# Performance work log

Hardware: AMD Instinct MI355X
Metric: run time of the kernel (lower is better)

Reference implementation:

```python
import math
import jax, jax.numpy as jnp
import numpy as np

B, P, L = 32, 128, 64
DIN, TE, H, NH, NL = 16, 64, 512, 8, 2
DH = H // NH
DP = DIN + TE
TAU = 300.0
DELTA = 300.0

_PARAM_SPEC = [
    ("te_scale_w", (1, 1)), ("te_scale_b", (1,)),
    ("te_per_w", (TE - 1, 1)), ("te_per_b", (TE - 1,)),
    ("inp_w", (H, DP)), ("inp_b", (H,)),
    ("wq", (H, H)), ("bq", (H,)), ("wk", (H, H)), ("bk", (H,)),
    ("wv", (H, H)), ("bv", (H,)), ("wo", (H, H)), ("bo", (H,)),
    ("ffn_w1", (H, H)), ("ffn_b1", (H,)), ("ffn_w2", (H, H)), ("ffn_b2", (H,)),
    ("ln1_g", (H,)), ("ln1_b", (H,)), ("ln2_g", (H,)), ("ln2_b", (H,)),
    ("exists_bias", (1, 1, H)),
    ("gwq", (NL, H, H)), ("gbq", (NL, H)), ("gwk", (NL, H, H)), ("gbk", (NL, H)),
    ("gwv", (NL, H, H)), ("gbv", (NL, H)), ("gwo", (NL, H, H)), ("gbo", (NL, H)),
]


def setup_inputs() -> dict:
    key = jax.random.key(0)
    ks = jax.random.split(key, 3 + len(_PARAM_SPEC))
    inp = {
        "x": jax.random.normal(ks[0], (B, P, L, DIN), jnp.float32),
        "tt": jax.random.uniform(ks[1], (B, P, L, 1), jnp.float32),
        "mask": jax.random.randint(ks[2], (B, P, L, 1), 0, 2).astype(jnp.int32),
    }
    for i, (name, shp) in enumerate(_PARAM_SPEC):
        inp[name] = 0.02 * jax.random.normal(ks[3 + i], shp, jnp.float32)
    # LayerNorm affine params: gamma=1, beta=0
    inp["ln1_g"] = jnp.ones((H,), jnp.float32)
    inp["ln1_b"] = jnp.zeros((H,), jnp.float32)
    inp["ln2_g"] = jnp.ones((H,), jnp.float32)
    inp["ln2_b"] = jnp.zeros((H,), jnp.float32)
    return inp


def _layernorm(x, g, b, eps=1e-5):
    m = x.mean(-1, keepdims=True)
    v = ((x - m) ** 2).mean(-1, keepdims=True)
    return (x - m) / jnp.sqrt(v + eps) * g + b


def _time_bias(m):
    idx = jnp.arange(m)
    dist = jnp.abs(idx[:, None] - idx[None, :]).astype(jnp.float32) * DELTA
    return jnp.log(jnp.exp(-dist / TAU) + 1e-12)  # [P, P]


def _pos_encoding(p, d):
    pos = jnp.arange(p, dtype=jnp.float32)[:, None]
    div = jnp.exp(jnp.arange(0, d, 2, dtype=jnp.float32) * (-math.log(10000.0) / d))
    pe = jnp.zeros((p, d), jnp.float32)
    pe = pe.at[:, 0::2].set(jnp.sin(pos * div))
    pe = pe.at[:, 1::2].set(jnp.cos(pos * div))
    return pe


def reference(x, tt, mask,
              te_scale_w, te_scale_b, te_per_w, te_per_b,
              inp_w, inp_b, wq, bq, wk, bk, wv, bv, wo, bo,
              ffn_w1, ffn_b1, ffn_w2, ffn_b2, ln1_g, ln1_b, ln2_g, ln2_b,
              exists_bias, gwq, gbq, gwk, gbk, gwv, gbv, gwo, gbo):
    b, p, l, _ = x.shape
    # --- Learnable time embedding: scale linear + sin(periodic linear), concat ---
    te1 = tt @ te_scale_w.T + te_scale_b                      # [B,P,L,1]
    te2 = jnp.sin(tt @ te_per_w.T + te_per_b)                 # [B,P,L,TE-1]
    pts = jnp.concatenate([x, te1, te2], axis=-1)             # [B,P,L,DP]

    valid = (mask[..., 0] > 0).reshape(b * p, l)              # [N,L] bool
    h = (pts.reshape(b * p, l, DP) @ inp_w.T) + inp_b         # [N,L,H]

    has_any = jnp.any(valid, axis=1)                          # [N]
    key_pad = ~valid
    # Empty patches: unmask position 0 and zero its features
    key_pad = key_pad.at[:, 0].set(key_pad[:, 0] & has_any)
    pos0 = (jnp.arange(l) == 0)[None, :, None]
    h = jnp.where((~has_any)[:, None, None] & pos0, 0.0, h)

    # --- Intra-patch MHA (GAT) ---
    def heads(t, w, bias):
        return ((t @ w.T) + bias).reshape(b * p, l, NH, DH)
    q, k, v = heads(h, wq, bq), heads(h, wk, bk), heads(h, wv, bv)
    sc = jnp.einsum("nqhd,nkhd->nhqk", q, k) / math.sqrt(DH)
    sc = jnp.where(key_pad[:, None, None, :], -1e9, sc)
    z = jnp.einsum("nhqk,nkhd->nqhd", jax.nn.softmax(sc, axis=-1), v)
    z = z.reshape(b * p, l, H) @ wo.T + bo
    h = _layernorm(h + z, ln1_g, ln1_b)
    ffn = jax.nn.relu(h @ ffn_w1.T + ffn_b1) @ ffn_w2.T + ffn_b2
    h = _layernorm(h + ffn, ln2_g, ln2_b)

    # Masked mean pooling -> patch tokens
    w = valid.astype(jnp.float32)[..., None]                  # [N,L,1]
    denom = jnp.clip(w.sum(axis=1), 1.0)
    h = ((h * w).sum(axis=1) / denom).reshape(b, p, H)        # [B,P,H]

    # Exists bias for missing patches + positional encoding
    pexists = has_any.reshape(b, p).astype(jnp.float32)       # [B,P]
    h = h + exists_bias * (1.0 - pexists)[..., None]
    h = h + _pos_encoding(p, H)[None]

    # --- Patch-level time-biased graph attention stack (residual) ---
    tb = _time_bias(p)[None, None]                            # [1,1,P,P]
    kp = (pexists <= 0.0)[:, None, None, :]                   # [B,1,1,P]
    for li in range(NL):
        def gh(t, w, bias):
            return ((t @ w.T) + bias).reshape(b, p, NH, DH)
        q = gh(h, gwq[li], gbq[li])
        k = gh(h, gwk[li], gbk[li])
        v = gh(h, gwv[li], gbv[li])
        att = jnp.einsum("bqhd,bkhd->bhqk", q, k) / math.sqrt(DH) + tb
        att = jnp.where(kp, -1e9, att)
        out = jnp.einsum("bhqk,bkhd->bqhd", jax.nn.softmax(att, axis=-1), v)
        out = out.reshape(b, p, H) @ gwo[li].T + gbo[li]
        out = out * pexists[..., None]
        h = h + out
    return h
```

## Files before the change

### kernel.cpp

```cpp
#include <hip/hip_runtime.h>

#define NTOK 4096
#define CH   512
#define NCHUNK 8

typedef _Float16 f16;
typedef __attribute__((ext_vector_type(8))) _Float16 half8;
typedef __attribute__((ext_vector_type(4))) _Float16 half4;
typedef __attribute__((ext_vector_type(4))) float f32x4;

#define OFF_INPW 0
#define OFF_WQKV (512*128)
#define OFF_WO   (OFF_WQKV + 3*512*512)
#define OFF_W1   (OFF_WO + 512*512)
#define OFF_W2   (OFF_W1 + 512*512)
#define OFF_GW   (OFF_W2 + 512*512)
#define WBF_TOT  (OFF_GW + 8*512*512)

static __device__ __forceinline__ f32x4 mfma16(half8 a, half8 b, f32x4 c){
  return __builtin_amdgcn_mfma_f32_16x16x32_f16(a, b, c, 0, 0, 0);
}

static __device__ __forceinline__ void gld_lds16(const f16* g, f16* l){
  __builtin_amdgcn_global_load_lds(
      (const __attribute__((address_space(1))) void*)g,
      (__attribute__((address_space(3))) void*)l, 16, 0, 0);
}

#define FULL_BARRIER() do { \
    asm volatile("" ::: "memory"); \
    __builtin_amdgcn_s_barrier(); \
    __builtin_amdgcn_sched_barrier(0); \
  } while(0)

__global__ __launch_bounds__(256) void conv_weights(
    const float* __restrict__ inpw, const float* __restrict__ wq, const float* __restrict__ wk,
    const float* __restrict__ wv, const float* __restrict__ wo, const float* __restrict__ w1,
    const float* __restrict__ w2, const float* __restrict__ gwq, const float* __restrict__ gwk,
    const float* __restrict__ gwv, const float* __restrict__ gwo, f16* __restrict__ wbf,
    const float* __restrict__ bq, const float* __restrict__ bk, const float* __restrict__ bv,
    const float* __restrict__ gbq, const float* __restrict__ gbk, const float* __restrict__ gbv,
    float* __restrict__ biasb)
{
  int e = blockIdx.x*256 + threadIdx.x;
  int y = blockIdx.y;
  if (y == 0){
    if (e < 512*128){
      int row = e>>7, col = e&127;
      float v = (col < 80) ? inpw[row*80 + col] : 0.f;
      wbf[OFF_INPW + e] = (f16)v;
    }
    return;
  }
  if (y == 15){
    if (e < 1536){
      biasb[e] = (e < 512) ? bq[e] : (e < 1024 ? bk[e-512] : bv[e-1024]);
    } else if (e < 3*1536){
      int idx = e - 1536, li = idx/1536, c = idx - li*1536;
      float v = (c < 512) ? gbq[li*512 + c] : (c < 1024 ? gbk[li*512 + c-512] : gbv[li*512 + c-1024]);
      biasb[e] = v;
    }
    return;
  }
  if (e >= 512*512) return;
  const float* src; int off;
  if (y <= 6){
    const float* tab[6] = {wq, wk, wv, wo, w1, w2};
    src = tab[y-1]; off = OFF_WQKV + (y-1)*512*512;
  } else {
    int idx = y-7; int li = idx>>2, part = idx&3;
    const float* tab[4] = {gwq, gwk, gwv, gwo};
    src = tab[part] + (size_t)li*512*512; off = OFF_GW + idx*512*512;
  }
  wbf[off + e] = (f16)src[e];
}

__global__ __launch_bounds__(256) void build_mask(
    const int* __restrict__ mask, float* __restrict__ mb, float* __restrict__ pex)
{
  int wv = threadIdx.x>>6, lane = threadIdx.x&63;
  int n = blockIdx.x*4 + wv;
  int valid = mask[(size_t)n*64 + lane] > 0;
  unsigned long long ball = __ballot(valid);
  int hasany = (ball != 0ull);
  int masked = (lane == 0) ? (!valid && hasany) : (!valid);
  mb[(size_t)n*64 + lane] = masked ? -1e9f : 0.f;
  if (lane == 0) pex[n] = hasany ? 1.f : 0.f;
}

__global__ __launch_bounds__(256) void pts_build(
    const float* __restrict__ x, const float* __restrict__ tt,
    const float* __restrict__ tsw, const float* __restrict__ tsb,
    const float* __restrict__ tpw, const float* __restrict__ tpb,
    f16* __restrict__ pts, int rowbase)
{
  int e = blockIdx.x*256 + threadIdx.x;
  int r = e>>7, col = e&127;
  size_t grow = (size_t)rowbase + r;
  float v;
  if (col < 16) v = x[grow*16 + col];
  else if (col >= 80) v = 0.f;
  else {
    float t = tt[grow];
    if (col == 16) v = t*tsw[0] + tsb[0];
    else           v = __sinf(t*tpw[col-17] + tpb[col-17]);
  }
  pts[e] = (f16)v;
}

template<int RESID, bool RELU, bool OUTF32, bool ZEMPTY>
__global__ __launch_bounds__(256) void gemm128(
    const f16* __restrict__ A, const f16* __restrict__ W, const float* __restrict__ bias,
    void* __restrict__ Cout, const void* __restrict__ Rsd, const float* __restrict__ pex,
    int K, int lda, int ldc, int nbase, f16* __restrict__ dual)
{
  __shared__ __align__(16) f16 As[128][64];
  __shared__ __align__(16) f16 Bs[128][64];
  const int tid = threadIdx.x;
  const int m0 = blockIdx.x*128, n0 = blockIdx.y*128;
  const int wv = tid>>6, lane = tid&63, l15 = lane&15, quad = lane>>4;
  const int wm = (wv&1)*64, wn = (wv>>1)*64;
  const int srow = lane>>3;
  const int schunk = (lane&7) ^ srow;
  f32x4 acc[4][4] = {};
  for (int kc = 0; kc < K; kc += 64){
    __syncthreads();
    #pragma unroll
    for (int i=0; i<4; i++){
      const int rA = wv*32 + i*8;
      gld_lds16(A + (size_t)(m0 + rA + srow)*lda + kc + schunk*8, &As[rA][0]);
      gld_lds16(W + (size_t)(n0 + rA + srow)*K   + kc + schunk*8, &Bs[rA][0]);
    }
    __syncthreads();
    #pragma unroll
    for (int kk=0; kk<2; kk++){
      half8 av[4], bv8[4];
      #pragma unroll
      for (int t=0; t<4; t++){
        const int ra = wm + t*16 + l15;
        av[t]  = *(const half8*)(&As[ra][(((kk*4 + quad) ^ (ra&7)))*8]);
        const int rb = wn + t*16 + l15;
        bv8[t] = *(const half8*)(&Bs[rb][(((kk*4 + quad) ^ (rb&7)))*8]);
      }
      #pragma unroll
      for (int mt=0; mt<4; mt++)
        #pragma unroll
        for (int nt=0; nt<4; nt++)
          acc[mt][nt] = mfma16(av[mt], bv8[nt], acc[mt][nt]);
    }
  }
  #pragma unroll
  for (int mt=0; mt<4; mt++){
    #pragma unroll
    for (int nt=0; nt<4; nt++){
      #pragma unroll
      for (int i=0; i<4; i++){
        int gr = m0 + wm + mt*16 + quad*4 + i;
        int gc = n0 + wn + nt*16 + l15;
        float v = acc[mt][nt][i] + bias[gc];
        if (RELU) v = fmaxf(v, 0.f);
        if (RESID == 1) v += (float)((const f16*)Rsd)[(size_t)gr*ldc + gc];
        if (ZEMPTY){ if ((gr&63)==0 && pex[nbase + (gr>>6)]==0.f) v = 0.f; }
        if (RESID == 2) v = v*pex[gr] + ((const float*)Rsd)[(size_t)gr*ldc + gc];
        if (OUTF32) ((float*)Cout)[(size_t)gr*ldc + gc] = v;
        else        ((f16*)Cout)[(size_t)gr*ldc + gc] = (f16)v;
        if (RESID == 2){ if (dual) dual[(size_t)gr*ldc + gc] = (f16)v; }
      }
    }
  }
}

template<int RESID, bool RELU>
__global__ __launch_bounds__(512,2) void gemm256(
    const f16* __restrict__ A, const f16* __restrict__ W, const float* __restrict__ bias,
    f16* __restrict__ Cout, const f16* __restrict__ Rsd,
    int K, int lda, int ldc)
{
  __shared__ __align__(16) f16 As[2*2*128*64];
  __shared__ __align__(16) f16 Bs[2*2*128*64];

  const int tid = threadIdx.x;
  const int wv = tid>>6, lane = tid&63, l15 = lane&15, quad = lane>>4;
  const int wm = wv>>2;
  const int wn = wv&3;

  const int gy = gridDim.y;
  int nwg = gridDim.x*gy;
  int orig = blockIdx.x*gy + blockIdx.y;
  int qq = nwg>>3;
  int swz = (orig&7)*qq + (orig>>3);
  const int m0 = (swz/gy)*256, n0 = (swz%gy)*256;

  const int NT = K>>6;

  auto stage_half = [&](int t, int hf){
    int tc = t < NT ? t : NT-1;
    int kc = tc<<6;
    int b  = t & 1;
    #pragma unroll
    for (int i=0;i<2;i++){
      int idx = wv*2+i;
      int row = idx*8 + (lane>>3);
      int col = kc + (((lane&7) ^ (lane>>3))<<3);
      if (hf < 2)
        gld_lds16(A + (size_t)(m0 + hf*128 + row)*lda + col,
                  As + b*16384 + hf*8192 + idx*512);
      else
        gld_lds16(W + (size_t)(n0 + (hf-2)*128 + row)*K + col,
                  Bs + b*16384 + (hf-2)*8192 + idx*512);
    }
  };
  auto ldsA = [&](int b, int mt, int kk)->half8{
    int r = mt*16 + l15;
    int g = kk*4 + quad;
    return *(const half8*)(As + b*16384 + wm*8192 + r*64 + ((g ^ (r&7))<<3));
  };
  auto ldsB = [&](int b, int nt, int kk)->half8{
    int r = (wn&1)*64 + nt*16 + l15;
    int g = kk*4 + quad;
    return *(const half8*)(Bs + b*16384 + (wn>>1)*8192 + r*64 + ((g ^ (r&7))<<3));
  };

  half8 a[8], b0[4], b1[4];
  f32x4 acc[8][4] = {};
  auto mm8 = [&](int mb, half8* bq, int nb){
    __builtin_amdgcn_s_setprio(1);
    #pragma unroll
    for (int m=0;m<4;m++)
      #pragma unroll
      for (int n=0;n<2;n++)
        #pragma unroll
        for (int k=0;k<2;k++)
          acc[mb+m][nb+n] = mfma16(a[m*2+k], bq[n*2+k], acc[mb+m][nb+n]);
    __builtin_amdgcn_s_setprio(0);
  };

  stage_half(0,0); stage_half(0,1); stage_half(0,2); stage_half(0,3);
  stage_half(1,2); stage_half(1,3);
  asm volatile("s_waitcnt vmcnt(4)" ::: "memory");
  FULL_BARRIER();

  for (int t = 0; t < NT; t += 2){
    #pragma unroll
    for (int hv = 0; hv < 2; hv++){
      const int c  = t + hv;
      const int bf = hv;
      #pragma unroll
      for (int m=0;m<4;m++){ a[m*2]=ldsA(bf,m,0); a[m*2+1]=ldsA(bf,m,1); }
      #pragma unroll
      for (int n=0;n<2;n++){ b0[n*2]=ldsB(bf,n,0); b0[n*2+1]=ldsB(bf,n,1); }
      stage_half(c+1, 0);
      FULL_BARRIER();
      mm8(0, b0, 0);
      FULL_BARRIER();
      #pragma unroll
      for (int n=0;n<2;n++){ b1[n*2]=ldsB(bf,n+2,0); b1[n*2+1]=ldsB(bf,n+2,1); }
      stage_half(c+1, 1);
      FULL_BARRIER();
      mm8(0, b1, 2);
      FULL_BARRIER();
      #pragma unroll
      for (int m=0;m<4;m++){ a[m*2]=ldsA(bf,m+4,0); a[m*2+1]=ldsA(bf,m+4,1); }
      stage_half(c+2, 2);
      FULL_BARRIER();
      mm8(4, b1, 2);
      FULL_BARRIER();
      stage_half(c+2, 3);
      asm volatile("s_waitcnt vmcnt(4)" ::: "memory");
      FULL_BARRIER();
      mm8(4, b0, 0);
      FULL_BARRIER();
    }
  }

  #pragma unroll
  for (int mt=0; mt<8; mt++){
    #pragma unroll
    for (int nt=0; nt<4; nt++){
      #pragma unroll
      for (int i=0; i<4; i++){
        int gr = m0 + wm*128 + mt*16 + quad*4 + i;
        int gc = n0 + wn*64  + nt*16 + l15;
        float v = acc[mt][nt][i] + bias[gc];
        if (RELU) v = fmaxf(v, 0.f);
        if (RESID == 1) v += (float)Rsd[(size_t)gr*ldc + gc];
        Cout[(size_t)gr*ldc + gc] = (f16)v;
      }
    }
  }
}

__global__ __launch_bounds__(128) void attn_patch(
    f16* __restrict__ qkv, const float* __restrict__ maskbias, int nbase)
{
  __shared__ f16 Vt[2][64][72];
  __shared__ f16 Ps[2][64][72];
  __shared__ float mbs[64];
  const int tid = threadIdx.x, wv = tid>>6, lane = tid&63, l15 = lane&15, quad = lane>>4;
  const int n = blockIdx.x, h = blockIdx.y*2 + wv;
  if (tid < 64) mbs[tid] = maskbias[(size_t)(nbase+n)*64 + tid];
  const f16* Vb = qkv + 1024 + h*64;
  for (int i=0; i<64; i++)
    Vt[wv][lane][i] = Vb[((size_t)n*64 + i)*1536 + lane];
  __syncthreads();
  const f16* Qb  = qkv + (size_t)n*64*1536 + h*64;
  const f16* Kbb = Qb + 512;
  f32x4 sacc[4][4] = {};
  #pragma unroll
  for (int kc=0; kc<2; kc++){
    half8 af[4], bf[4];
    #pragma unroll
    for (int t4=0; t4<4; t4++){
      af[t4] = *(const half8*)(Qb  + (size_t)(t4*16 + l15)*1536 + kc*32 + quad*8);
      bf[t4] = *(const half8*)(Kbb + (size_t)(t4*16 + l15)*1536 + kc*32 + quad*8);
    }
    #pragma unroll
    for (int ti=0; ti<4; ti++)
      #pragma unroll
      for (int tj=0; tj<4; tj++)
        sacc[ti][tj] = mfma16(af[ti], bf[tj], sacc[ti][tj]);
  }
  #pragma unroll
  for (int ti=0; ti<4; ti++){
    #pragma unroll
    for (int i=0; i<4; i++){
      float mx = -1e30f;
      #pragma unroll
      for (int tj=0; tj<4; tj++){
        float sv = sacc[ti][tj][i]*0.125f + mbs[tj*16 + l15];
        sacc[ti][tj][i] = sv;
        mx = fmaxf(mx, sv);
      }
      #pragma unroll
      for (int off=1; off<16; off<<=1) mx = fmaxf(mx, __shfl_xor(mx, off, 64));
      float sum = 0.f;
      #pragma unroll
      for (int tj=0; tj<4; tj++){
        float pv = __expf(sacc[ti][tj][i] - mx);
        sacc[ti][tj][i] = pv; sum += pv;
      }
      #pragma unroll
      for (int off=1; off<16; off<<=1) sum += __shfl_xor(sum, off, 64);
      float inv = 1.f/sum;
      int q = ti*16 + quad*4 + i;
      #pragma unroll
      for (int tj=0; tj<4; tj++)
        Ps[wv][q][tj*16 + l15] = (f16)(sacc[ti][tj][i]*inv);
    }
  }
  __syncthreads();
  f32x4 zacc[4][4] = {};
  #pragma unroll
  for (int kc=0; kc<2; kc++){
    half8 va[4], pb[4];
    #pragma unroll
    for (int t4=0; t4<4; t4++){
      va[t4] = *(const half8*)(&Vt[wv][t4*16 + l15][kc*32 + quad*8]);
      pb[t4] = *(const half8*)(&Ps[wv][t4*16 + l15][kc*32 + quad*8]);
    }
    #pragma unroll
    for (int ti2=0; ti2<4; ti2++)
      #pragma unroll
      for (int tj=0; tj<4; tj++)
        zacc[ti2][tj] = mfma16(va[ti2], pb[tj], zacc[ti2][tj]);
  }
  __syncthreads();
  #pragma unroll
  for (int ti2=0; ti2<4; ti2++)
    #pragma unroll
    for (int tj=0; tj<4; tj++){
      int q = tj*16 + l15, d0 = ti2*16 + quad*4;
      half4 pk;
      #pragma unroll
      for (int i=0; i<4; i++) pk[i] = (f16)zacc[ti2][tj][i];
      *(half4*)(&Vt[wv][q][d0]) = pk;
    }
  __syncthreads();
  #pragma unroll
  for (int i=0; i<8; i++){
    int q = i*8 + (lane>>3), d0 = (lane&7)*8;
    *(uint4*)(qkv + ((size_t)n*64 + q)*1536 + h*64 + d0) = *(const uint4*)(&Vt[wv][q][d0]);
  }
}

__global__ __launch_bounds__(256) void ln_rows(
    const f16* __restrict__ X, f16* __restrict__ Y,
    const float* __restrict__ g, const float* __restrict__ b)
{
  int wv = threadIdx.x>>6, lane = threadIdx.x&63;
  size_t row = (size_t)blockIdx.x*4 + wv;
  half8 raw = *(const half8*)(X + row*512 + lane*8);
  float xv[8];
  #pragma unroll
  for (int j=0; j<8; j++) xv[j] = (float)raw[j];
  float s = 0.f;
  #pragma unroll
  for (int j=0; j<8; j++) s += xv[j];
  #pragma unroll
  for (int off=1; off<64; off<<=1) s += __shfl_xor(s, off, 64);
  float mean = s*(1.f/512.f);
  float vs = 0.f;
  #pragma unroll
  for (int j=0; j<8; j++){ float d = xv[j]-mean; vs += d*d; }
  #pragma unroll
  for (int off=1; off<64; off<<=1) vs += __shfl_xor(vs, off, 64);
  float rstd = rsqrtf(vs*(1.f/512.f) + 1e-5f);
  half8 o;
  #pragma unroll
  for (int j=0; j<8; j++){
    int c = lane*8 + j;
    o[j] = (f16)((xv[j]-mean)*rstd*g[c] + b[c]);
  }
  *(half8*)(Y + row*512 + lane*8) = o;
}

__global__ __launch_bounds__(256) void pool_ln2(
    const f16* __restrict__ X, const int* __restrict__ mask,
    const float* __restrict__ g, const float* __restrict__ b, const float* __restrict__ eb,
    float* __restrict__ out, f16* __restrict__ hcopy, int nbase)
{
  __shared__ float mArr[64], rArr[64], vArr[64];
  const int tid = threadIdx.x, wv = tid>>6, lane = tid&63;
  const int n = blockIdx.x, ng = nbase + n, p = ng & 127;
  for (int j=0; j<16; j++){
    int l = wv*16 + j;
    half8 raw = *(const half8*)(X + ((size_t)n*64 + l)*512 + lane*8);
    float s=0.f, ss=0.f;
    #pragma unroll
    for (int jj=0; jj<8; jj++){ float f = (float)raw[jj]; s += f; ss += f*f; }
    #pragma unroll
    for (int off=1; off<64; off<<=1){ s += __shfl_xor(s, off, 64); ss += __shfl_xor(ss, off, 64); }
    if (lane == 0){
      float m = s*(1.f/512.f);
      mArr[l] = m; rArr[l] = rsqrtf(ss*(1.f/512.f) - m*m + 1e-5f);
    }
  }
  if (tid < 64) vArr[tid] = (mask[(size_t)ng*64 + tid] > 0) ? 1.f : 0.f;
  __syncthreads();
  float cnt = 0.f;
  #pragma unroll
  for (int l=0; l<64; l++) cnt += vArr[l];
  float denom = fmaxf(cnt, 1.f);
  float pexv = cnt > 0.f ? 1.f : 0.f;
  float a0=0.f, a1=0.f;
  for (int l=0; l<64; l++){
    float wgt = vArr[l], m = mArr[l], rs = rArr[l];
    float x0 = (float)X[((size_t)n*64+l)*512 + tid];
    float x1 = (float)X[((size_t)n*64+l)*512 + tid + 256];
    a0 += wgt*(x0-m)*rs; a1 += wgt*(x1-m)*rs;
  }
  #pragma unroll
  for (int k=0; k<2; k++){
    int c = tid + k*256;
    float acc = k ? a1 : a0;
    float fr = __expf(-(float)(c & ~1) * (9.210340371976184f/512.f));
    float ang = (float)p * fr;
    float pe = (c & 1) ? cosf(ang) : sinf(ang);
    float o = (g[c]*acc + b[c]*cnt)/denom + eb[c]*(1.f - pexv) + pe;
    out[(size_t)ng*512 + c] = o;
    hcopy[(size_t)ng*512 + c] = (f16)o;
  }
}

__global__ __launch_bounds__(256) void attn_graph(
    f16* __restrict__ qkv, const float* __restrict__ pexists)
{
  __shared__ f16 Vt[64][136];
  __shared__ f16 Ps[4][32][136];
  __shared__ float pxs[128];
  const int tid = threadIdx.x, wv = tid>>6, lane = tid&63, l15 = lane&15, quad = lane>>4;
  const int b = blockIdx.x, h = blockIdx.y;
  if (tid < 128) pxs[tid] = pexists[b*128 + tid];
  const f16* Vb = qkv + 1024 + h*64;
  for (int i=0; i<32; i++){
    int e = tid + i*256, k = e>>6, d = e&63;
    Vt[d][k] = Vb[((size_t)b*128 + k)*1536 + d];
  }
  __syncthreads();
  const f16* Qb = qkv + h*64;
  const f16* Kb = qkv + 512 + h*64;
  const int qb = wv*32;
  f32x4 sacc[2][8] = {};
  #pragma unroll
  for (int kc=0; kc<2; kc++){
    half8 af[2], bf[8];
    #pragma unroll
    for (int ti=0; ti<2; ti++)
      af[ti] = *(const half8*)(Qb + ((size_t)b*128 + qb + ti*16 + l15)*1536 + kc*32 + quad*8);
    #pragma unroll
    for (int tj=0; tj<8; tj++)
      bf[tj] = *(const half8*)(Kb + ((size_t)b*128 + tj*16 + l15)*1536 + kc*32 + quad*8);
    #pragma unroll
    for (int ti=0; ti<2; ti++)
      #pragma unroll
      for (int tj=0; tj<8; tj++)
        sacc[ti][tj] = mfma16(af[ti], bf[tj], sacc[ti][tj]);
  }
  #pragma unroll
  for (int ti=0; ti<2; ti++){
    #pragma unroll
    for (int i=0; i<4; i++){
      int q = qb + ti*16 + quad*4 + i;
      float mx = -1e30f;
      #pragma unroll
      for (int tj=0; tj<8; tj++){
        int col = tj*16 + l15;
        int dd = q - col; if (dd < 0) dd = -dd;
        float tb = __logf(__expf(-(float)dd) + 1e-12f);
        float sv = sacc[ti][tj][i]*0.125f + tb + (pxs[col] > 0.f ? 0.f : -1e9f);
        sacc[ti][tj][i] = sv;
        mx = fmaxf(mx, sv);
      }
      #pragma unroll
      for (int off=1; off<16; off<<=1) mx = fmaxf(mx, __shfl_xor(mx, off, 64));
      float sum = 0.f;
      #pragma unroll
      for (int tj=0; tj<8; tj++){
        float pv = __expf(sacc[ti][tj][i] - mx);
        sacc[ti][tj][i] = pv; sum += pv;
      }
      #pragma unroll
      for (int off=1; off<16; off<<=1) sum += __shfl_xor(sum, off, 64);
      float inv = 1.f/sum;
      int ql = ti*16 + quad*4 + i;
      #pragma unroll
      for (int tj=0; tj<8; tj++)
        Ps[wv][ql][tj*16 + l15] = (f16)(sacc[ti][tj][i]*inv);
    }
  }
  __syncthreads();
  f32x4 zacc[4][2] = {};
  #pragma unroll
  for (int kc=0; kc<4; kc++){
    half8 va[4], pb[2];
    #pragma unroll
    for (int ti2=0; ti2<4; ti2++)
      va[ti2] = *(const half8*)(&Vt[ti2*16 + l15][kc*32 + quad*8]);
    #pragma unroll
    for (int tjq=0; tjq<2; tjq++)
      pb[tjq] = *(const half8*)(&Ps[wv][tjq*16 + l15][kc*32 + quad*8]);
    #pragma unroll
    for (int ti2=0; ti2<4; ti2++)
      #pragma unroll
      for (int tjq=0; tjq<2; tjq++)
        zacc[ti2][tjq] = mfma16(va[ti2], pb[tjq], zacc[ti2][tjq]);
  }
  __syncthreads();
  #pragma unroll
  for (int ti2=0; ti2<4; ti2++)
    #pragma unroll
    for (int tjq=0; tjq<2; tjq++){
      int ql = tjq*16 + l15, d0 = ti2*16 + quad*4;
      half4 pk;
      #pragma unroll
      for (int i=0; i<4; i++) pk[i] = (f16)zacc[ti2][tjq][i];
      *(half4*)(&Ps[wv][ql][d0]) = pk;
    }
  __syncthreads();
  {
    int q = tid>>1, hf = tid&1;
    const f16* src = &Ps[q>>5][q&31][hf*32];
    #pragma unroll
    for (int j=0; j<4; j++)
      *(uint4*)(qkv + ((size_t)b*128 + q)*1536 + h*64 + hf*32 + j*8) = *(const uint4*)(src + j*8);
  }
}

extern "C" void kernel_launch(void* const* d_in, const int* in_sizes, int n_in,
                              void* d_out, int out_size, void* d_ws, size_t ws_size,
                              hipStream_t stream)
{
  (void)in_sizes; (void)n_in; (void)out_size; (void)ws_size;
  const float* x    = (const float*)d_in[0];
  const float* tt   = (const float*)d_in[1];
  const int*   mask = (const int*)  d_in[2];
  const float* tsw  = (const float*)d_in[3];
  const float* tsb  = (const float*)d_in[4];
  const float* tpw  = (const float*)d_in[5];
  const float* tpb  = (const float*)d_in[6];
  const float* inpw = (const float*)d_in[7];
  const float* inpb = (const float*)d_in[8];
  const float* wq   = (const float*)d_in[9];
  const float* bq   = (const float*)d_in[10];
  const float* wk   = (const float*)d_in[11];
  const float* bk   = (const float*)d_in[12];
  const float* wv   = (const float*)d_in[13];
  const float* bv   = (const float*)d_in[14];
  const float* wo   = (const float*)d_in[15];
  const float* bo   = (const float*)d_in[16];
  const float* w1   = (const float*)d_in[17];
  const float* b1   = (const float*)d_in[18];
  const float* w2   = (const float*)d_in[19];
  const float* b2   = (const float*)d_in[20];
  const float* ln1g = (const float*)d_in[21];
  const float* ln1b = (const float*)d_in[22];
  const float* ln2g = (const float*)d_in[23];
  const float* ln2b = (const float*)d_in[24];
  const float* eb   = (const float*)d_in[25];
  const float* gwq  = (const float*)d_in[26];
  const float* gbq  = (const float*)d_in[27];
  const float* gwk  = (const float*)d_in[28];
  const float* gbk  = (const float*)d_in[29];
  const float* gwv  = (const float*)d_in[30];
  const float* gbv  = (const float*)d_in[31];
  const float* gwo  = (const float*)d_in[32];
  const float* gbo  = (const float*)d_in[33];
  float* out = (float*)d_out;

  char* wp = (char*)d_ws;
  auto alloc = [&](size_t bytes)->char*{
    char* p = wp; wp += (bytes + 255) & ~(size_t)255; return p;
  };
  f16*   wbf   = (f16*)  alloc((size_t)WBF_TOT*2);
  float* mb    = (float*)alloc((size_t)NTOK*64*4);
  float* pex   = (float*)alloc((size_t)NTOK*4);
  float* biasb = (float*)alloc((size_t)3*1536*4);
  f16*   ptsb  = (f16*)  alloc((size_t)CH*64*128*2);
  f16*   bufA  = (f16*)  alloc((size_t)CH*64*512*2);
  f16*   bufB  = (f16*)  alloc((size_t)CH*64*512*2);
  f16*   bufC  = (f16*)  alloc((size_t)CH*64*512*2);
  f16*   qkv   = (f16*)  alloc((size_t)CH*64*1536*2);
  f16*   hbf   = (f16*)  alloc((size_t)NTOK*512*2);

  conv_weights<<<dim3(1024,16),256,0,stream>>>(inpw,wq,wk,wv,wo,w1,w2,gwq,gwk,gwv,gwo,wbf,
                                               bq,bk,bv,gbq,gbk,gbv,biasb);
  build_mask<<<NTOK/4,256,0,stream>>>(mask, mb, pex);

  const int MB  = CH*64/128;
  const int MB2 = CH*64/256;
  for (int ch=0; ch<NCHUNK; ch++){
    int nbase = ch*CH;
    int rowbase = nbase*64;
    pts_build<<<CH*64*128/256,256,0,stream>>>(x,tt,tsw,tsb,tpw,tpb,ptsb,rowbase);
    gemm128<0,false,false,true ><<<dim3(MB,4),256,0,stream>>>(ptsb, wbf+OFF_INPW, inpb, bufA, nullptr, pex, 128, 128, 512, nbase, nullptr);
    gemm256<0,false><<<dim3(MB2,6),512,0,stream>>>(bufA, wbf+OFF_WQKV, biasb, qkv, nullptr, 512, 512, 1536);
    attn_patch<<<dim3(CH,4),128,0,stream>>>(qkv, mb, nbase);
    gemm256<1,false><<<dim3(MB2,2),512,0,stream>>>(qkv, wbf+OFF_WO, bo, bufA, bufA, 512, 1536, 512);
    ln_rows<<<CH*64/4,256,0,stream>>>(bufA, bufB, ln1g, ln1b);
    gemm256<0,true ><<<dim3(MB2,2),512,0,stream>>>(bufB, wbf+OFF_W1, b1, bufC, nullptr, 512, 512, 512);
    gemm256<1,false><<<dim3(MB2,2),512,0,stream>>>(bufC, wbf+OFF_W2, b2, bufB, bufB, 512, 512, 512);
    pool_ln2<<<CH,256,0,stream>>>(bufB, mask, ln2g, ln2b, eb, out, hbf, nbase);
  }

  f16* qkvg = bufB;
  for (int li=0; li<2; li++){
    gemm128<0,false,false,false><<<dim3(32,12),256,0,stream>>>(hbf, wbf+OFF_GW + (size_t)li*4*512*512, biasb + 1536*(1+li), qkvg, nullptr, nullptr, 512, 512, 1536, 0, nullptr);
    attn_graph<<<dim3(32,8),256,0,stream>>>(qkvg, pex);
    gemm128<2,false,true ,false><<<dim3(32,4),256,0,stream>>>(qkvg, wbf+OFF_GW + (size_t)(li*4+3)*512*512, gbo+li*512, out, out, pex, 512, 1536, 512, 0, (li==0)? hbf : nullptr);
  }
}
```

Measured before the change: 2.300 ms.

## Run 256x256 GEMM with 16 waves per block and reschedule K-loop staging

The 256-tile GEMM moves from 8 to 16 waves per block, so each wave now owns a 64x64 output sub-tile instead of 128x64. This halves the accumulator and fragment registers per wave. The K-loop is reordered: the A and B halves are staged at different points, with one global-to-LDS load per wave per half, and the vmcnt waits are adjusted to match. The aim is more waves to hide latency and lower register pressure. In exchange there are more barriers across 16 waves and less MFMA work per LDS read.

```diff
diff --git a/kernel.cpp b/kernel.cpp
--- a/kernel.cpp
+++ b/kernel.cpp
@@ -171,7 +171,7 @@
 }
 
 template<int RESID, bool RELU>
-__global__ __launch_bounds__(512,2) void gemm256(
+__global__ __launch_bounds__(1024,4) void gemm256(
     const f16* __restrict__ A, const f16* __restrict__ W, const float* __restrict__ bias,
     f16* __restrict__ Cout, const f16* __restrict__ Rsd,
     int K, int lda, int ldc)
@@ -197,23 +197,19 @@
     int tc = t < NT ? t : NT-1;
     int kc = tc<<6;
     int b  = t & 1;
-    #pragma unroll
-    for (int i=0;i<2;i++){
-      int idx = wv*2+i;
-      int row = idx*8 + (lane>>3);
-      int col = kc + (((lane&7) ^ (lane>>3))<<3);
-      if (hf < 2)
-        gld_lds16(A + (size_t)(m0 + hf*128 + row)*lda + col,
-                  As + b*16384 + hf*8192 + idx*512);
-      else
-        gld_lds16(W + (size_t)(n0 + (hf-2)*128 + row)*K + col,
-                  Bs + b*16384 + (hf-2)*8192 + idx*512);
-    }
+    int row = wv*8 + (lane>>3);
+    int col = kc + (((lane&7) ^ (lane>>3))<<3);
+    if (hf < 2)
+      gld_lds16(A + (size_t)(m0 + hf*128 + row)*lda + col,
+                As + b*16384 + hf*8192 + wv*512);
+    else
+      gld_lds16(W + (size_t)(n0 + (hf-2)*128 + row)*K + col,
+                Bs + b*16384 + (hf-2)*8192 + wv*512);
   };
   auto ldsA = [&](int b, int mt, int kk)->half8{
-    int r = mt*16 + l15;
+    int r = (wm&1)*64 + mt*16 + l15;
     int g = kk*4 + quad;
-    return *(const half8*)(As + b*16384 + wm*8192 + r*64 + ((g ^ (r&7))<<3));
+    return *(const half8*)(As + b*16384 + (wm>>1)*8192 + r*64 + ((g ^ (r&7))<<3));
   };
   auto ldsB = [&](int b, int nt, int kk)->half8{
     int r = (wn&1)*64 + nt*16 + l15;
@@ -221,23 +217,21 @@
     return *(const half8*)(Bs + b*16384 + (wn>>1)*8192 + r*64 + ((g ^ (r&7))<<3));
   };
 
-  half8 a[8], b0[4], b1[4];
-  f32x4 acc[8][4] = {};
-  auto mm8 = [&](int mb, half8* bq, int nb){
+  half8 a4[4], bA[2], bB[2];
+  f32x4 acc[4][4] = {};
+  auto mm8 = [&](half8* bp, int nb){
     __builtin_amdgcn_s_setprio(1);
     #pragma unroll
     for (int m=0;m<4;m++)
       #pragma unroll
       for (int n=0;n<2;n++)
-        #pragma unroll
-        for (int k=0;k<2;k++)
-          acc[mb+m][nb+n] = mfma16(a[m*2+k], bq[n*2+k], acc[mb+m][nb+n]);
+        acc[m][nb+n] = mfma16(a4[m], bp[n], acc[m][nb+n]);
     __builtin_amdgcn_s_setprio(0);
   };
 
   stage_half(0,0); stage_half(0,1); stage_half(0,2); stage_half(0,3);
-  stage_half(1,2); stage_half(1,3);
-  asm volatile("s_waitcnt vmcnt(4)" ::: "memory");
+  stage_half(1,0); stage_half(1,1);
+  asm volatile("s_waitcnt vmcnt(2)" ::: "memory");
   FULL_BARRIER();
 
   for (int t = 0; t < NT; t += 2){
@@ -246,41 +240,41 @@
       const int c  = t + hv;
       const int bf = hv;
       #pragma unroll
-      for (int m=0;m<4;m++){ a[m*2]=ldsA(bf,m,0); a[m*2+1]=ldsA(bf,m,1); }
-      #pragma unroll
-      for (int n=0;n<2;n++){ b0[n*2]=ldsB(bf,n,0); b0[n*2+1]=ldsB(bf,n,1); }
-      stage_half(c+1, 0);
-      FULL_BARRIER();
-      mm8(0, b0, 0);
-      FULL_BARRIER();
-      #pragma unroll
-      for (int n=0;n<2;n++){ b1[n*2]=ldsB(bf,n+2,0); b1[n*2+1]=ldsB(bf,n+2,1); }
-      stage_half(c+1, 1);
-      FULL_BARRIER();
-      mm8(0, b1, 2);
-      FULL_BARRIER();
-      #pragma unroll
-      for (int m=0;m<4;m++){ a[m*2]=ldsA(bf,m+4,0); a[m*2+1]=ldsA(bf,m+4,1); }
-      stage_half(c+2, 2);
-      FULL_BARRIER();
-      mm8(4, b1, 2);
-      FULL_BARRIER();
-      stage_half(c+2, 3);
-      asm volatile("s_waitcnt vmcnt(4)" ::: "memory");
-      FULL_BARRIER();
-      mm8(4, b0, 0);
-      FULL_BARRIER();
-    }
-  }
-
-  #pragma unroll
-  for (int mt=0; mt<8; mt++){
+      for (int m=0;m<4;m++) a4[m] = ldsA(bf, m, 0);
+      bA[0] = ldsB(bf, 0, 0); bA[1] = ldsB(bf, 1, 0);
+      stage_half(c+1, 2);
+      stage_half(c+1, 3);
+      FULL_BARRIER();
+      mm8(bA, 0);
+      FULL_BARRIER();
+      bB[0] = ldsB(bf, 2, 0); bB[1] = ldsB(bf, 3, 0);
+      FULL_BARRIER();
+      mm8(bB, 2);
+      FULL_BARRIER();
+      #pragma unroll
+      for (int m=0;m<4;m++) a4[m] = ldsA(bf, m, 1);
+      bA[0] = ldsB(bf, 0, 1); bA[1] = ldsB(bf, 1, 1);
+      FULL_BARRIER();
+      mm8(bA, 0);
+      FULL_BARRIER();
+      bB[0] = ldsB(bf, 2, 1); bB[1] = ldsB(bf, 3, 1);
+      stage_half(c+2, 0);
+      stage_half(c+2, 1);
+      asm volatile("s_waitcnt vmcnt(2)" ::: "memory");
+      FULL_BARRIER();
+      mm8(bB, 2);
+      FULL_BARRIER();
+    }
+  }
+
+  #pragma unroll
+  for (int mt=0; mt<4; mt++){
     #pragma unroll
     for (int nt=0; nt<4; nt++){
       #pragma unroll
       for (int i=0; i<4; i++){
-        int gr = m0 + wm*128 + mt*16 + quad*4 + i;
-        int gc = n0 + wn*64  + nt*16 + l15;
+        int gr = m0 + wm*64 + mt*16 + quad*4 + i;
+        int gc = n0 + wn*64 + nt*16 + l15;
         float v = acc[mt][nt][i] + bias[gc];
         if (RELU) v = fmaxf(v, 0.f);
         if (RESID == 1) v += (float)Rsd[(size_t)gr*ldc + gc];
@@ -633,12 +627,12 @@
     int rowbase = nbase*64;
     pts_build<<<CH*64*128/256,256,0,stream>>>(x,tt,tsw,tsb,tpw,tpb,ptsb,rowbase);
     gemm128<0,false,false,true ><<<dim3(MB,4),256,0,stream>>>(ptsb, wbf+OFF_INPW, inpb, bufA, nullptr, pex, 128, 128, 512, nbase, nullptr);
-    gemm256<0,false><<<dim3(MB2,6),512,0,stream>>>(bufA, wbf+OFF_WQKV, biasb, qkv, nullptr, 512, 512, 1536);
+    gemm256<0,false><<<dim3(MB2,6),1024,0,stream>>>(bufA, wbf+OFF_WQKV, biasb, qkv, nullptr, 512, 512, 1536);
     attn_patch<<<dim3(CH,4),128,0,stream>>>(qkv, mb, nbase);
-    gemm256<1,false><<<dim3(MB2,2),512,0,stream>>>(qkv, wbf+OFF_WO, bo, bufA, bufA, 512, 1536, 512);
+    gemm256<1,false><<<dim3(MB2,2),1024,0,stream>>>(qkv, wbf+OFF_WO, bo, bufA, bufA, 512, 1536, 512);
     ln_rows<<<CH*64/4,256,0,stream>>>(bufA, bufB, ln1g, ln1b);
-    gemm256<0,true ><<<dim3(MB2,2),512,0,stream>>>(bufB, wbf+OFF_W1, b1, bufC, nullptr, 512, 512, 512);
-    gemm256<1,false><<<dim3(MB2,2),512,0,stream>>>(bufC, wbf+OFF_W2, b2, bufB, bufB, 512, 512, 512);
+    gemm256<0,true ><<<dim3(MB2,2),1024,0,stream>>>(bufB, wbf+OFF_W1, b1, bufC, nullptr, 512, 512, 512);
+    gemm256<1,false><<<dim3(MB2,2),1024,0,stream>>>(bufC, wbf+OFF_W2, b2, bufB, bufB, 512, 512, 512);
     pool_ln2<<<CH,256,0,stream>>>(bufB, mask, ln2g, ln2b, eb, out, hbf, nbase);
   }
 
```

New measurement: 2.376 ms. 1.03x slower.
